# Performance work log

Hardware: AMD Instinct MI355X
Metric: run time of the kernel (lower is better)

Reference implementation:

```python
import jax, jax.numpy as jnp
import numpy as np

BATCH = 4096
IN_F = 1024
OUT_F = 1024
GRID_SIZE = 8
SPLINE_ORDER = 3
SCALE_SPLINE = 1.0


def setup_inputs() -> dict:
    key = jax.random.key(0)
    kx, kb, ks = jax.random.split(key, 3)
    # inputs live on the spline domain [-1, 1]
    x = jax.random.uniform(kx, (BATCH, IN_F), jnp.float32, -1.0, 1.0)
    # kaiming_uniform_(a=sqrt(5)) on (out,in) -> U(-1/sqrt(in), 1/sqrt(in))
    bound = 1.0 / float(np.sqrt(IN_F))
    base_weight = jax.random.uniform(kb, (OUT_F, IN_F), jnp.float32, -bound, bound)
    # normal(mean=0, std=0.1), (out, in, grid_size + spline_order)
    spline_weight = 0.1 * jax.random.normal(ks, (OUT_F, IN_F, GRID_SIZE + SPLINE_ORDER), jnp.float32)
    # uniform knot vector with spacing h = 2/grid_size over [-1,1], extended by
    # spline_order knots on each side so Cox-de Boor yields grid_size+spline_order bases
    h = 2.0 / GRID_SIZE
    grid = jnp.arange(-SPLINE_ORDER, GRID_SIZE + SPLINE_ORDER + 1, dtype=jnp.float32) * h - 1.0
    return {"x": x, "base_weight": base_weight, "spline_weight": spline_weight, "grid": grid}


def b_spline_basis(x, grid, k):
    # x: (batch, in), grid: (grid_size + 2k + 1,) shared across (out, in) pairs
    xe = x[..., None]  # (b, i, 1)
    # degree-0: indicator of knot interval -> (b, i, grid_size + 2k)
    basis = ((xe >= grid[:-1]) & (xe < grid[1:])).astype(x.dtype)
    for d in range(1, k + 1):  # Cox-de Boor recursion up to degree k
        left_denom = grid[d:-1] - grid[:-(d + 1)]
        right_denom = grid[d + 1:] - grid[1:-d]
        left_denom = jnp.where(left_denom > 0, left_denom, 1.0)
        right_denom = jnp.where(right_denom > 0, right_denom, 1.0)
        basis = ((xe - grid[:-(d + 1)]) / left_denom * basis[..., :-1]
                 + (grid[d + 1:] - xe) / right_denom * basis[..., 1:])
    return basis  # (b, i, grid_size + k)


def reference(x, base_weight, spline_weight, grid):
    base_output = x @ base_weight.T  # (b, out)
    basis = b_spline_basis(x, grid, SPLINE_ORDER)  # (b, i, L), L = grid_size + k
    # grid is identical for every (out, in) pair, so the per-(o,i) basis of the
    # original collapses to a per-i basis; einsum 'bil,oil->bo' is the same math.
    spline_output = jnp.einsum('bil,oil->bo', basis, spline_weight)
    return base_output + SCALE_SPLINE * spline_output
```

## Files before the change

### kernel.cpp

```cpp
#include <hip/hip_runtime.h>
#include <hip/hip_bf16.h>
#include <cstdint>

#define BATCH 4096
#define INF   1024
#define OUTF  1024
#define LCH   12
#define KTOT  (INF*LCH)

#define BM 128
#define BN 128
#define IC 8
#define BK (IC*LCH)
#define NCHUNK (INF/IC)
#define NGRAN 12
#define THREADS 512
#define BUFSZ (NGRAN*128*8)

typedef __bf16 bf16x8 __attribute__((ext_vector_type(8)));
typedef float  f32x4  __attribute__((ext_vector_type(4)));
typedef unsigned long long ull;

struct alignas(16) U2 { ull x, y; };

__device__ __forceinline__ unsigned short f2bf(float f) {
  unsigned int u = __builtin_bit_cast(unsigned int, f);
  u += 0x7FFFu + ((u >> 16) & 1u);
  return (unsigned short)(u >> 16);
}

__device__ __forceinline__ void async_copy16(const void* g, void* l) {
  __builtin_amdgcn_global_load_lds(
      (const __attribute__((address_space(1))) unsigned int*)g,
      (__attribute__((address_space(3))) unsigned int*)l,
      16, 0, 0);
}

#define PIPE_BARRIER() do {                                        \
  asm volatile("s_waitcnt vmcnt(4) lgkmcnt(0)" ::: "memory");      \
  __builtin_amdgcn_sched_barrier(0);                               \
  __builtin_amdgcn_s_barrier();                                    \
  __builtin_amdgcn_sched_barrier(0);                               \
} while (0)

__global__ __launch_bounds__(256) void kan_build_wt(
    const float* __restrict__ sw,
    const float* __restrict__ bw,
    unsigned short* __restrict__ Wt)
{
  int idx = blockIdx.x * 256 + threadIdx.x;
  int o = idx >> 10;
  int i = idx & 1023;
  const float* s = sw + (size_t)(o * 1024 + i) * 11;
  unsigned short v[12];
#pragma unroll
  for (int l = 0; l < 11; ++l) v[l] = f2bf(s[l]);
  v[11] = f2bf(bw[o * 1024 + i]);
  unsigned short* d = Wt + (size_t)o * KTOT + i * 12;
  *reinterpret_cast<ushort4*>(d + 0) = make_ushort4(v[0], v[1], v[2],  v[3]);
  *reinterpret_cast<ushort4*>(d + 4) = make_ushort4(v[4], v[5], v[6],  v[7]);
  *reinterpret_cast<ushort4*>(d + 8) = make_ushort4(v[8], v[9], v[10], v[11]);
}

__global__ __launch_bounds__(THREADS, 1) void kan_gemm(
    const float* __restrict__ x,
    const unsigned short* __restrict__ Wt,
    float* __restrict__ out)
{
  __shared__ alignas(16) unsigned short smem[5 * BUFSZ];

  const int tid  = threadIdx.x;
  const int lane = tid & 63;
  const int wid  = tid >> 6;
  const int wm   = (wid >> 1) * 32;
  const int wn   = (wid & 1) * 64;
  const int bm   = (int)blockIdx.x >> 3;
  const int bn   = (int)blockIdx.x & 7;
  const int lr   = lane & 15;
  const int lk   = lane >> 4;

  const int ab  = tid & 127;
  const int ai0 = (tid >> 7) << 1;
  const float* xrow = x + (size_t)(bm * BM + ab) * INF + ai0;

  unsigned short* Bcur = smem;
  unsigned short* Bnxt = smem + BUFSZ;
  unsigned short* Bnn  = smem + 2 * BUFSZ;
  unsigned short* Acur = smem + 3 * BUFSZ;
  unsigned short* Aalt = smem + 4 * BUFSZ;

  f32x4 acc[2][4] = {};

  auto stageB = [&](int c, unsigned short* Bd) {
#pragma unroll
    for (int qq = 0; qq < 3; ++qq) {
      int G  = (wid * 3 + qq) * 64 + lane;
      int kk = G >> 7;
      int oo = G & 127;
      const unsigned short* src = Wt + (size_t)(bn * BN + oo) * KTOT + (c * BK + kk * 8);
      async_copy16(src, Bd + (wid * 3 + qq) * 512);
    }
  };

  auto buildA = [&](float2 xv, unsigned short* Ad) {
    ull W[6];
#pragma unroll
    for (int j = 0; j < 2; ++j) {
      float xx = (j == 0) ? xv.x : xv.y;
      float u  = fmaf(xx, 4.0f, 7.0f);
      float fm = floorf(u);
      int   mi = (int)fm;
      float t  = u - fm;
      float s  = 1.0f - t;
      float t2 = t * t, t3 = t2 * t;
      float w0 = (s * s * s) * (1.0f / 6.0f);
      float w3 = t3 * (1.0f / 6.0f);
      float w1 = fmaf(0.5f, t3, 2.0f / 3.0f) - t2;
      float w2 = 1.0f - w0 - w1 - w3;
      int ls = mi - 3;

      ull W64 = (ull)f2bf(w0)
              | ((ull)f2bf(w1) << 16)
              | ((ull)f2bf(w2) << 32)
              | ((ull)f2bf(w3) << 48);
      int sh = ls << 4;
      int a  = sh & 63;
      ull lop  = W64 << a;
      ull hip_ = a ? (W64 >> (64 - a)) : 0ull;
      W[3 * j + 0] = (sh < 64) ? lop : 0ull;
      W[3 * j + 1] = (sh < 64) ? hip_ : lop;
      W[3 * j + 2] = ((sh < 64) ? 0ull : hip_) | ((ull)f2bf(xx) << 48);
    }
    U2* p = reinterpret_cast<U2*>(Ad);
    const int g0 = (ai0 >> 1) * 3;
    U2 u0; u0.x = W[0]; u0.y = W[1];
    U2 u1; u1.x = W[2]; u1.y = W[3];
    U2 u2; u2.x = W[4]; u2.y = W[5];
    p[(g0 + 0) * 128 + ab] = u0;
    p[(g0 + 1) * 128 + ab] = u1;
    p[(g0 + 2) * 128 + ab] = u2;
  };

  float2 x0v = *reinterpret_cast<const float2*>(xrow);
  stageB(0, Bcur);
  buildA(x0v, Acur);
  float2 xa = *reinterpret_cast<const float2*>(xrow + IC);
  stageB(1, Bnxt);
  PIPE_BARRIER();

  for (int c = 0; c < NCHUNK; ++c) {
    int cf = (c + 2 < NCHUNK) ? (c + 2) : (NCHUNK - 1);
    float2 xb = *reinterpret_cast<const float2*>(xrow + cf * IC);
    stageB(cf, Bnn);
    buildA(xa, Aalt);

#pragma unroll
    for (int kk32 = 0; kk32 < 3; ++kk32) {
      bf16x8 af[2], bfr[4];
#pragma unroll
      for (int mf = 0; mf < 2; ++mf)
        af[mf] = *reinterpret_cast<const bf16x8*>(
            &Acur[(((kk32 * 4 + lk) * 128) + (wm + mf * 16 + lr)) * 8]);
#pragma unroll
      for (int nf = 0; nf < 4; ++nf)
        bfr[nf] = *reinterpret_cast<const bf16x8*>(
            &Bcur[(((kk32 * 4 + lk) * 128) + (wn + nf * 16 + lr)) * 8]);
#pragma unroll
      for (int mf = 0; mf < 2; ++mf)
#pragma unroll
        for (int nf = 0; nf < 4; ++nf)
          acc[mf][nf] = __builtin_amdgcn_mfma_f32_16x16x32_bf16(
              af[mf], bfr[nf], acc[mf][nf], 0, 0, 0);
    }

    PIPE_BARRIER();

    unsigned short* t = Bcur; Bcur = Bnxt; Bnxt = Bnn; Bnn = t;
    t = Acur; Acur = Aalt; Aalt = t;
    xa = xb;
  }

#pragma unroll
  for (int mf = 0; mf < 2; ++mf) {
#pragma unroll
    for (int v = 0; v < 4; ++v) {
      int row = bm * BM + wm + mf * 16 + lk * 4 + v;
      float* orow = out + (size_t)row * OUTF + bn * BN + wn + lr;
#pragma unroll
      for (int nf = 0; nf < 4; ++nf)
        orow[nf * 16] = acc[mf][nf][v];
    }
  }
}

extern "C" void kernel_launch(void* const* d_in, const int* in_sizes, int n_in,
                              void* d_out, int out_size, void* d_ws, size_t ws_size,
                              hipStream_t stream) {
  const float* x  = (const float*)d_in[0];
  const float* bw = (const float*)d_in[1];
  const float* sw = (const float*)d_in[2];
  float* out = (float*)d_out;

  unsigned short* Wt = (unsigned short*)d_ws;
  if (ws_size < (size_t)OUTF * KTOT * sizeof(unsigned short)) return;

  kan_build_wt<<<(OUTF * INF) / 256, 256, 0, stream>>>(sw, bw, Wt);
  kan_gemm<<<(BATCH / BM) * (OUTF / BN), THREADS, 0, stream>>>(x, Wt, out);
}
```

Measured before the change: 166.0 us.

## Split K-chunk into ping-pong phases with barriers and MFMA priority

Restructures the main loop so each of the three k-substeps becomes a separate phase: LDS fragment reads, then a barrier, then an lgkm wait, then MFMAs raised to high priority, then another barrier. This is a ping-pong style schedule meant to keep waves in lockstep so memory and MFMA phases interleave across waves. The spline-basis build now runs between the first and second MFMA phase, with finer vmcnt waits. The extra barriers per chunk (six instead of one) add synchronisation overhead. With one block of 8 waves per CU there is little inter-block overlap to gain.

```diff
diff --git a/kernel.cpp b/kernel.cpp
--- a/kernel.cpp
+++ b/kernel.cpp
@@ -36,12 +36,17 @@
       16, 0, 0);
 }
 
-#define PIPE_BARRIER() do {                                        \
-  asm volatile("s_waitcnt vmcnt(4) lgkmcnt(0)" ::: "memory");      \
-  __builtin_amdgcn_sched_barrier(0);                               \
-  __builtin_amdgcn_s_barrier();                                    \
+#define WAIT_VM(N) do {                                            \
+  asm volatile("s_waitcnt vmcnt(" #N ")" ::: "memory");            \
   __builtin_amdgcn_sched_barrier(0);                               \
 } while (0)
+
+#define WAIT_LGKM0() do {                                          \
+  asm volatile("s_waitcnt lgkmcnt(0)" ::: "memory");               \
+  __builtin_amdgcn_sched_barrier(0);                               \
+} while (0)
+
+#define BARRIER() __builtin_amdgcn_s_barrier()
 
 __global__ __launch_bounds__(256) void kan_build_wt(
     const float* __restrict__ sw,
@@ -141,44 +146,66 @@
     p[(g0 + 2) * 128 + ab] = u2;
   };
 
+  bf16x8 af[2], bfr[4];
+  auto readFrags = [&](int kk32) {
+#pragma unroll
+    for (int mf = 0; mf < 2; ++mf)
+      af[mf] = *reinterpret_cast<const bf16x8*>(
+          &Acur[(((kk32 * 4 + lk) * 128) + (wm + mf * 16 + lr)) * 8]);
+#pragma unroll
+    for (int nf = 0; nf < 4; ++nf)
+      bfr[nf] = *reinterpret_cast<const bf16x8*>(
+          &Bcur[(((kk32 * 4 + lk) * 128) + (wn + nf * 16 + lr)) * 8]);
+  };
+  auto doMFMA = [&]() {
+    __builtin_amdgcn_s_setprio(1);
+#pragma unroll
+    for (int mf = 0; mf < 2; ++mf)
+#pragma unroll
+      for (int nf = 0; nf < 4; ++nf)
+        acc[mf][nf] = __builtin_amdgcn_mfma_f32_16x16x32_bf16(
+            af[mf], bfr[nf], acc[mf][nf], 0, 0, 0);
+    __builtin_amdgcn_s_setprio(0);
+  };
+
   float2 x0v = *reinterpret_cast<const float2*>(xrow);
   stageB(0, Bcur);
   buildA(x0v, Acur);
   float2 xa = *reinterpret_cast<const float2*>(xrow + IC);
   stageB(1, Bnxt);
-  PIPE_BARRIER();
+  asm volatile("s_waitcnt vmcnt(4) lgkmcnt(0)" ::: "memory");
+  __builtin_amdgcn_sched_barrier(0);
+  BARRIER();
 
   for (int c = 0; c < NCHUNK; ++c) {
     int cf = (c + 2 < NCHUNK) ? (c + 2) : (NCHUNK - 1);
     float2 xb = *reinterpret_cast<const float2*>(xrow + cf * IC);
     stageB(cf, Bnn);
+    WAIT_VM(8);
+    readFrags(0);
+    BARRIER();
+    WAIT_LGKM0();
+    doMFMA();
+    BARRIER();
+    WAIT_VM(4);
     buildA(xa, Aalt);
-
-#pragma unroll
-    for (int kk32 = 0; kk32 < 3; ++kk32) {
-      bf16x8 af[2], bfr[4];
-#pragma unroll
-      for (int mf = 0; mf < 2; ++mf)
-        af[mf] = *reinterpret_cast<const bf16x8*>(
-            &Acur[(((kk32 * 4 + lk) * 128) + (wm + mf * 16 + lr)) * 8]);
-#pragma unroll
-      for (int nf = 0; nf < 4; ++nf)
-        bfr[nf] = *reinterpret_cast<const bf16x8*>(
-            &Bcur[(((kk32 * 4 + lk) * 128) + (wn + nf * 16 + lr)) * 8]);
-#pragma unroll
-      for (int mf = 0; mf < 2; ++mf)
-#pragma unroll
-        for (int nf = 0; nf < 4; ++nf)
-          acc[mf][nf] = __builtin_amdgcn_mfma_f32_16x16x32_bf16(
-              af[mf], bfr[nf], acc[mf][nf], 0, 0, 0);
-    }
-
-    PIPE_BARRIER();
+    readFrags(1);
+    BARRIER();
+    WAIT_LGKM0();
+    doMFMA();
+    BARRIER();
+    readFrags(2);
+    BARRIER();
+    WAIT_LGKM0();
+    doMFMA();
+    BARRIER();
 
     unsigned short* t = Bcur; Bcur = Bnxt; Bnxt = Bnn; Bnn = t;
     t = Acur; Acur = Aalt; Aalt = t;
     xa = xb;
   }
+
+  asm volatile("s_waitcnt vmcnt(0) lgkmcnt(0)" ::: "memory");
 
 #pragma unroll
   for (int mf = 0; mf < 2; ++mf) {
```

After: 226.4 us. +36.4%, slower.
